# Kernel tuning notes

Hardware: AMD Instinct MI355X
Metric: run time of the kernel (lower is better)

## Reference

```python
import jax, jax.numpy as jnp
import numpy as np

BATCH = 4096
DIM = 256
TEMPERATURE = 0.5
EPS = 1e-8  # torch CosineSimilarity norm clamp


def setup_inputs() -> dict:
    key = jax.random.key(0)
    k1, k2 = jax.random.split(key)
    zA = jax.random.normal(k1, (BATCH, DIM), dtype=jnp.float32)
    zB = jax.random.normal(k2, (BATCH, DIM), dtype=jnp.float32)
    return {"zA": zA, "zB": zB}


def reference(zA, zB):
    b = zA.shape[0]
    N = 2 * b
    z = jnp.concatenate([zA, zB], axis=0)                      # [N, D]
    norm = jnp.maximum(jnp.linalg.norm(z, axis=1, keepdims=True), EPS)
    zn = z / norm
    # cosine-similarity matrix via normalize + GEMM (same math as the
    # broadcasted CosineSimilarity(dim=2) in the original)
    sim = (zn @ zn.T) / TEMPERATURE                            # [N, N]

    idx = jnp.arange(N)
    pos = sim[idx, (idx + b) % N]                              # diag(+b) ++ diag(-b)

    # CE with label 0 over logits=[pos, negatives]; the logit set per row is
    # exactly {all j != i} (pos partner included once), so mask only the diagonal.
    neg_inf = jnp.finfo(sim.dtype).min
    masked = jnp.where(jnp.eye(N, dtype=bool), neg_inf, sim)
    per_row = jax.nn.logsumexp(masked, axis=1) - pos           # [N]
    loss = jnp.sum(per_row) / N                                # reduction='sum' / N
    return loss
```

## Files before the change

### kernel.cpp

```cpp
#include <hip/hip_runtime.h>
#include <hip/hip_bf16.h>

#define N_ROWS 8192
#define BATCH 4096
#define DIM 256

#define NB 64
#define BR 128
#define CT 32
#define NT 4
#define NBLK (NB * (NB + 1) / 2)
#define TILEB (CT * 512)
#define KEXP 2.8853900817779268f

typedef __attribute__((ext_vector_type(8))) short bfrag8;
typedef __attribute__((ext_vector_type(4))) float facc4;

#define GLOAD_LDS16(g, l) __builtin_amdgcn_global_load_lds( \
    (const __attribute__((address_space(1))) unsigned int*)(g), \
    (__attribute__((address_space(3))) unsigned int*)(l), 16, 0, 0)

__global__ __launch_bounds__(256) void normalize_kernel(
    const float* __restrict__ zA, const float* __restrict__ zB,
    __hip_bfloat16* __restrict__ zn) {
    int tid = threadIdx.x;
    int wave = tid >> 6, lane = tid & 63;
    int row = blockIdx.x * 4 + wave;
    const float* src = (row < BATCH) ? (zA + (size_t)row * DIM)
                                     : (zB + (size_t)(row - BATCH) * DIM);
    float4 v = ((const float4*)src)[lane];
    float ss = v.x * v.x + v.y * v.y + v.z * v.z + v.w * v.w;
    #pragma unroll
    for (int m = 32; m; m >>= 1) ss += __shfl_xor(ss, m);
    float inv = 1.0f / fmaxf(sqrtf(ss), 1e-8f);
    union { ushort4 u; __hip_bfloat16 h[4]; } o;
    o.h[0] = __float2bfloat16(v.x * inv);
    o.h[1] = __float2bfloat16(v.y * inv);
    o.h[2] = __float2bfloat16(v.z * inv);
    o.h[3] = __float2bfloat16(v.w * inv);
    ((ushort4*)zn)[(size_t)row * (DIM / 4) + lane] = o.u;
}

__global__ __launch_bounds__(256, 3) void ntxent_main(
    const __hip_bfloat16* __restrict__ zn_,
    float* __restrict__ ep, float* __restrict__ pp) {
    const char* zn = (const char*)zn_;
    __shared__ char lds[2 * TILEB] __attribute__((aligned(1024)));
    __shared__ float colbuf[4][BR];
    int tid = threadIdx.x, lane = tid & 63, wave = tid >> 6;
    int quad = lane >> 4, l15 = lane & 15;

    int bid = blockIdx.x;
    int k = (bid & 7) * (NBLK / 8) + (bid >> 3);

    int bi = (int)(0.5f * (129.0f - sqrtf(16641.0f - 8.0f * (float)k)));
    if (bi < 0) bi = 0;
    if (bi > NB - 1) bi = NB - 1;
    while (bi * (129 - bi) / 2 > k) --bi;
    while ((bi + 1) * (128 - bi) / 2 <= k) ++bi;
    int bj = bi + (k - bi * (129 - bi) / 2);
    bool diagblk = (bi == bj);

    int row0 = bi * BR + wave * 32;
    const char* gBt = zn + (size_t)bj * BR * 512;

    int h = lane >> 5;
    int olane = (lane & 31) * 16;
    unsigned sofs[4];
    #pragma unroll
    for (int c = 0; c < 4; c++) {
        int col = wave * 8 + 2 * c + h;
        sofs[c] = (unsigned)(col * 512 + (olane ^ ((col & 7) << 4)));
    }

    #pragma unroll
    for (int c = 0; c < 4; c++)
        GLOAD_LDS16(gBt + sofs[c], lds + wave * 4096 + c * 1024);

    bfrag8 a[2][8];
    #pragma unroll
    for (int s = 0; s < 2; s++) {
        const char* ap = zn + (size_t)(row0 + s * 16 + l15) * 512 + quad * 16;
        #pragma unroll
        for (int ks = 0; ks < 8; ks++)
            a[s][ks] = *(const bfrag8*)(ap + ks * 64);
    }

    float es[2][4];
    #pragma unroll
    for (int s = 0; s < 2; s++)
        #pragma unroll
        for (int r = 0; r < 4; r++) es[s][r] = 0.f;

    __syncthreads();

    for (int t = 0; t < NT; t++) {
        char* cur = lds + (t & 1) * TILEB;
        char* nxt = lds + ((t + 1) & 1) * TILEB;
        if (t + 1 < NT) {
            const char* g = gBt + (size_t)(t + 1) * TILEB;
            #pragma unroll
            for (int c = 0; c < 4; c++)
                GLOAD_LDS16(g + sofs[c], nxt + wave * 4096 + c * 1024);
        }

        #pragma unroll
        for (int sub = 0; sub < 2; sub++) {
            int c2 = sub * 16 + l15;
            const char* bp = cur + c2 * 512;
            unsigned sw = (unsigned)((c2 & 7) << 4);
            bfrag8 bf[8];
            #pragma unroll
            for (int ks = 0; ks < 8; ks++) {
                unsigned o = (unsigned)(quad * 16 + ks * 64);
                bf[ks] = *(const bfrag8*)(bp + (o ^ sw));
            }

            facc4 acc[2];
            acc[0] = (facc4){0.f, 0.f, 0.f, 0.f};
            acc[1] = (facc4){0.f, 0.f, 0.f, 0.f};
            #pragma unroll
            for (int ks = 0; ks < 8; ks++) {
                acc[0] = __builtin_amdgcn_mfma_f32_16x16x32_bf16(a[0][ks], bf[ks], acc[0], 0, 0, 0);
                acc[1] = __builtin_amdgcn_mfma_f32_16x16x32_bf16(a[1][ks], bf[ks], acc[1], 0, 0, 0);
            }

            int ctile = bj * BR + t * CT + sub * 16;
            int gcol = ctile + l15;
            float ce = 0.0f;
            bool isdiag = (ctile >> 5) == (row0 >> 5);
            bool ispos  = (ctile >> 5) == ((row0 ^ BATCH) >> 5);

            if (isdiag) {
                #pragma unroll
                for (int s = 0; s < 2; s++)
                    #pragma unroll
                    for (int r = 0; r < 4; r++) {
                        int grow = row0 + s * 16 + quad * 4 + r;
                        float e = __builtin_amdgcn_exp2f(acc[s][r] * KEXP);
                        if (gcol == grow) e = 0.0f;
                        es[s][r] += e; ce += e;
                    }
            } else {
                #pragma unroll
                for (int s = 0; s < 2; s++)
                    #pragma unroll
                    for (int r = 0; r < 4; r++) {
                        float e = __builtin_amdgcn_exp2f(acc[s][r] * KEXP);
                        es[s][r] += e; ce += e;
                    }
                if (ispos) {
                    #pragma unroll
                    for (int s = 0; s < 2; s++)
                        #pragma unroll
                        for (int r = 0; r < 4; r++) {
                            int grow = row0 + s * 16 + quad * 4 + r;
                            if (gcol == (grow ^ BATCH)) {
                                float d = acc[s][r];
                                pp[grow] = d;
                                pp[grow ^ BATCH] = d;
                            }
                        }
                }
            }
            if (!diagblk) {
                ce += __shfl_xor(ce, 16);
                ce += __shfl_xor(ce, 32);
                if (lane < 16) colbuf[wave][t * CT + sub * 16 + l15] = ce;
            }
        }

        __syncthreads();
    }

    #pragma unroll
    for (int s = 0; s < 2; s++)
        #pragma unroll
        for (int r = 0; r < 4; r++) {
            float e = es[s][r];
            #pragma unroll
            for (int m = 1; m < 16; m <<= 1) e += __shfl_xor(e, m);
            if (l15 == 0)
                ep[(size_t)(row0 + s * 16 + quad * 4 + r) * NB + bj] = e;
        }

    if (!diagblk && tid < BR) {
        float v = colbuf[0][tid] + colbuf[1][tid] + colbuf[2][tid] + colbuf[3][tid];
        ep[(size_t)(bj * BR + tid) * NB + bi] = v;
    }
}

__global__ __launch_bounds__(256) void finalize_kernel(
    const float* __restrict__ ep, const float* __restrict__ pp,
    float* __restrict__ out) {
    int tid = threadIdx.x;
    int i = blockIdx.x * 256 + tid;
    const float4* epr = (const float4*)(ep + (size_t)i * NB);
    float e = 0.0f;
    #pragma unroll
    for (int s = 0; s < NB / 4; s++) {
        float4 v = epr[s];
        e += (v.x + v.y) + (v.z + v.w);
    }
    float v = __logf(e) - 2.0f * pp[i];
    #pragma unroll
    for (int m = 32; m; m >>= 1) v += __shfl_xor(v, m);
    __shared__ float wsum[4];
    if ((tid & 63) == 0) wsum[tid >> 6] = v;
    __syncthreads();
    if (tid == 0)
        atomicAdd(out, (wsum[0] + wsum[1] + wsum[2] + wsum[3]) * (1.0f / N_ROWS));
}

extern "C" void kernel_launch(void* const* d_in, const int* in_sizes, int n_in,
                              void* d_out, int out_size, void* d_ws, size_t ws_size,
                              hipStream_t stream) {
    const float* zA = (const float*)d_in[0];
    const float* zB = (const float*)d_in[1];
    float* out = (float*)d_out;
    char* ws = (char*)d_ws;
    __hip_bfloat16* zn = (__hip_bfloat16*)ws;
    float* ep = (float*)(ws + (size_t)N_ROWS * DIM * 2);
    float* pp = ep + (size_t)N_ROWS * NB;

    hipMemsetAsync(out, 0, sizeof(float), stream);
    normalize_kernel<<<N_ROWS / 4, 256, 0, stream>>>(zA, zB, zn);
    ntxent_main<<<NBLK, 256, 0, stream>>>(zn, ep, pp);
    finalize_kernel<<<N_ROWS / 256, 256, 0, stream>>>(ep, pp, out);
}
```

Measured before the change: 105.3 us.

## Split fused GEMM+exp reduction into GEMM writing exp tiles and separate sum kernel

The fused kernel did the row and column exp-sum reductions in registers and LDS. It now writes every 128x128 exp tile to a workspace buffer in global memory. A new kernel then reads each tile back and computes row and column sums into the partial-sum array. This drops the shuffle and LDS reduction work from the GEMM kernel. In exchange it writes and rereads about 2080*64KB (roughly 136MB) of intermediate data and adds one more kernel launch.

```diff
diff --git a/kernel.cpp b/kernel.cpp
--- a/kernel.cpp
+++ b/kernel.cpp
@@ -19,6 +19,15 @@
 #define GLOAD_LDS16(g, l) __builtin_amdgcn_global_load_lds( \
     (const __attribute__((address_space(1))) unsigned int*)(g), \
     (__attribute__((address_space(3))) unsigned int*)(l), 16, 0, 0)
+
+__device__ __forceinline__ void pair_decode(int k, int& bi, int& bj) {
+    bi = (int)(0.5f * (129.0f - sqrtf(16641.0f - 8.0f * (float)k)));
+    if (bi < 0) bi = 0;
+    if (bi > NB - 1) bi = NB - 1;
+    while (bi * (129 - bi) / 2 > k) --bi;
+    while ((bi + 1) * (128 - bi) / 2 <= k) ++bi;
+    bj = bi + (k - bi * (129 - bi) / 2);
+}
 
 __global__ __launch_bounds__(256) void normalize_kernel(
     const float* __restrict__ zA, const float* __restrict__ zB,
@@ -41,28 +50,23 @@
     ((ushort4*)zn)[(size_t)row * (DIM / 4) + lane] = o.u;
 }
 
-__global__ __launch_bounds__(256, 3) void ntxent_main(
+__global__ __launch_bounds__(256, 3) void ntxent_gemm(
     const __hip_bfloat16* __restrict__ zn_,
-    float* __restrict__ ep, float* __restrict__ pp) {
+    float* __restrict__ E, float* __restrict__ pp) {
     const char* zn = (const char*)zn_;
     __shared__ char lds[2 * TILEB] __attribute__((aligned(1024)));
-    __shared__ float colbuf[4][BR];
     int tid = threadIdx.x, lane = tid & 63, wave = tid >> 6;
     int quad = lane >> 4, l15 = lane & 15;
 
     int bid = blockIdx.x;
     int k = (bid & 7) * (NBLK / 8) + (bid >> 3);
-
-    int bi = (int)(0.5f * (129.0f - sqrtf(16641.0f - 8.0f * (float)k)));
-    if (bi < 0) bi = 0;
-    if (bi > NB - 1) bi = NB - 1;
-    while (bi * (129 - bi) / 2 > k) --bi;
-    while ((bi + 1) * (128 - bi) / 2 <= k) ++bi;
-    int bj = bi + (k - bi * (129 - bi) / 2);
+    int bi, bj; pair_decode(k, bi, bj);
     bool diagblk = (bi == bj);
+    bool posblk  = (bj == (bi ^ 32));
 
     int row0 = bi * BR + wave * 32;
     const char* gBt = zn + (size_t)bj * BR * 512;
+    float* Et = E + (size_t)k * (BR * BR);
 
     int h = lane >> 5;
     int olane = (lane & 31) * 16;
@@ -85,12 +89,6 @@
         for (int ks = 0; ks < 8; ks++)
             a[s][ks] = *(const bfrag8*)(ap + ks * 64);
     }
-
-    float es[2][4];
-    #pragma unroll
-    for (int s = 0; s < 2; s++)
-        #pragma unroll
-        for (int r = 0; r < 4; r++) es[s][r] = 0.f;
 
     __syncthreads();
 
@@ -125,68 +123,84 @@
                 acc[1] = __builtin_amdgcn_mfma_f32_16x16x32_bf16(a[1][ks], bf[ks], acc[1], 0, 0, 0);
             }
 
-            int ctile = bj * BR + t * CT + sub * 16;
-            int gcol = ctile + l15;
-            float ce = 0.0f;
-            bool isdiag = (ctile >> 5) == (row0 >> 5);
-            bool ispos  = (ctile >> 5) == ((row0 ^ BATCH) >> 5);
-
-            if (isdiag) {
-                #pragma unroll
-                for (int s = 0; s < 2; s++)
+            int C = t * CT + sub * 16 + l15;
+            #pragma unroll
+            for (int s = 0; s < 2; s++) {
+                int R0 = wave * 32 + s * 16 + quad * 4;
+                int dd = C - R0;
+                if (posblk) {
                     #pragma unroll
-                    for (int r = 0; r < 4; r++) {
-                        int grow = row0 + s * 16 + quad * 4 + r;
-                        float e = __builtin_amdgcn_exp2f(acc[s][r] * KEXP);
-                        if (gcol == grow) e = 0.0f;
-                        es[s][r] += e; ce += e;
-                    }
-            } else {
-                #pragma unroll
-                for (int s = 0; s < 2; s++)
-                    #pragma unroll
-                    for (int r = 0; r < 4; r++) {
-                        float e = __builtin_amdgcn_exp2f(acc[s][r] * KEXP);
-                        es[s][r] += e; ce += e;
-                    }
-                if (ispos) {
-                    #pragma unroll
-                    for (int s = 0; s < 2; s++)
-                        #pragma unroll
-                        for (int r = 0; r < 4; r++) {
-                            int grow = row0 + s * 16 + quad * 4 + r;
-                            if (gcol == (grow ^ BATCH)) {
-                                float d = acc[s][r];
-                                pp[grow] = d;
-                                pp[grow ^ BATCH] = d;
-                            }
+                    for (int r = 0; r < 4; r++)
+                        if (dd == r) {
+                            int grow = bi * BR + R0 + r;
+                            float d = acc[s][r];
+                            pp[grow] = d;
+                            pp[grow ^ BATCH] = d;
                         }
                 }
+                float e0 = __builtin_amdgcn_exp2f(acc[s][0] * KEXP);
+                float e1 = __builtin_amdgcn_exp2f(acc[s][1] * KEXP);
+                float e2 = __builtin_amdgcn_exp2f(acc[s][2] * KEXP);
+                float e3 = __builtin_amdgcn_exp2f(acc[s][3] * KEXP);
+                if (diagblk) {
+                    e0 = (dd == 0) ? 0.0f : e0;
+                    e1 = (dd == 1) ? 0.0f : e1;
+                    e2 = (dd == 2) ? 0.0f : e2;
+                    e3 = (dd == 3) ? 0.0f : e3;
+                }
+                *(float4*)(Et + (size_t)C * BR + R0) = make_float4(e0, e1, e2, e3);
             }
-            if (!diagblk) {
-                ce += __shfl_xor(ce, 16);
-                ce += __shfl_xor(ce, 32);
-                if (lane < 16) colbuf[wave][t * CT + sub * 16 + l15] = ce;
-            }
-        }
-
+        }
         __syncthreads();
     }
-
-    #pragma unroll
-    for (int s = 0; s < 2; s++)
-        #pragma unroll
-        for (int r = 0; r < 4; r++) {
-            float e = es[s][r];
-            #pragma unroll
-            for (int m = 1; m < 16; m <<= 1) e += __shfl_xor(e, m);
-            if (l15 == 0)
-                ep[(size_t)(row0 + s * 16 + quad * 4 + r) * NB + bj] = e;
-        }
-
-    if (!diagblk && tid < BR) {
-        float v = colbuf[0][tid] + colbuf[1][tid] + colbuf[2][tid] + colbuf[3][tid];
-        ep[(size_t)(bj * BR + tid) * NB + bi] = v;
+}
+
+__global__ __launch_bounds__(256) void ntxent_sums(
+    const float* __restrict__ E, float* __restrict__ ep) {
+    int bid = blockIdx.x;
+    int k = (bid & 7) * (NBLK / 8) + (bid >> 3);
+    int bi, bj; pair_decode(k, bi, bj);
+    bool diagblk = (bi == bj);
+    const float* T = E + (size_t)k * (BR * BR);
+    int tid = threadIdx.x;
+
+    {
+        int C = tid >> 1, h = tid & 1;
+        const float4* p = (const float4*)(T + (size_t)C * BR + h * 64);
+        float cs = 0.0f;
+        #pragma unroll
+        for (int i = 0; i < 16; i++) {
+            float4 v = p[i];
+            cs += (v.x + v.y) + (v.z + v.w);
+        }
+        cs += __shfl_xor(cs, 1);
+        if (!diagblk && h == 0)
+            ep[(size_t)(bj * BR + C) * NB + bi] = cs;
+    }
+
+    {
+        int rg = tid >> 3, cc = tid & 7;
+        float r0 = 0.f, r1 = 0.f, r2 = 0.f, r3 = 0.f;
+        #pragma unroll
+        for (int i = 0; i < 16; i++) {
+            int C = cc * 16 + i;
+            float4 v = *(const float4*)(T + (size_t)C * BR + rg * 4);
+            r0 += v.x; r1 += v.y; r2 += v.z; r3 += v.w;
+        }
+        #pragma unroll
+        for (int m = 1; m < 8; m <<= 1) {
+            r0 += __shfl_xor(r0, m);
+            r1 += __shfl_xor(r1, m);
+            r2 += __shfl_xor(r2, m);
+            r3 += __shfl_xor(r3, m);
+        }
+        if (cc == 0) {
+            size_t base = (size_t)(bi * BR + rg * 4) * NB + bj;
+            ep[base] = r0;
+            ep[base + NB] = r1;
+            ep[base + 2 * NB] = r2;
+            ep[base + 3 * NB] = r3;
+        }
     }
 }
 
@@ -222,9 +236,11 @@
     __hip_bfloat16* zn = (__hip_bfloat16*)ws;
     float* ep = (float*)(ws + (size_t)N_ROWS * DIM * 2);
     float* pp = ep + (size_t)N_ROWS * NB;
+    float* E  = (float*)(ws + ((size_t)8 << 20));
 
     hipMemsetAsync(out, 0, sizeof(float), stream);
     normalize_kernel<<<N_ROWS / 4, 256, 0, stream>>>(zA, zB, zn);
-    ntxent_main<<<NBLK, 256, 0, stream>>>(zn, ep, pp);
+    ntxent_gemm<<<NBLK, 256, 0, stream>>>(zn, E, pp);
+    ntxent_sums<<<NBLK, 256, 0, stream>>>(E, ep);
     finalize_kernel<<<N_ROWS / 256, 256, 0, stream>>>(ep, pp, out);
 }
```

Result: slower. 152.6 us (+45.0%).

## Use 256x128 rectangular tiles over symmetric similarity triangle with paired row-band scheduling

Applied to the files above, without the earlier changes.

Each block now covers 256 rows by 128 columns instead of 128x128. Each wave holds 64 rows of A fragments in registers, so every LDS-loaded B fragment feeds four MFMAs instead of two. Blocks are scheduled as paired row bands to balance the triangular work, and the finalize kernel sums only the valid per-band partial entries. This raises register use, so occupancy drops from 3 to 2 blocks per CU, and the diagonal and positive-pair masking become per-element index checks.

```diff
diff --git a/kernel.cpp b/kernel.cpp
--- a/kernel.cpp
+++ b/kernel.cpp
@@ -5,11 +5,13 @@
 #define BATCH 4096
 #define DIM 256
 
-#define NB 64
-#define BR 128
+#define NP 32
+#define PR 256
+#define CW 128
+#define NJ 64
 #define CT 32
 #define NT 4
-#define NBLK (NB * (NB + 1) / 2)
+#define NBLK 1056
 #define TILEB (CT * 512)
 #define KEXP 2.8853900817779268f
 
@@ -41,54 +43,56 @@
     ((ushort4*)zn)[(size_t)row * (DIM / 4) + lane] = o.u;
 }
 
-__global__ __launch_bounds__(256, 3) void ntxent_main(
+__global__ __launch_bounds__(256, 2) void ntxent_main(
     const __hip_bfloat16* __restrict__ zn_,
     float* __restrict__ ep, float* __restrict__ pp) {
     const char* zn = (const char*)zn_;
     __shared__ char lds[2 * TILEB] __attribute__((aligned(1024)));
-    __shared__ float colbuf[4][BR];
+    __shared__ float colbuf[4][CW];
     int tid = threadIdx.x, lane = tid & 63, wave = tid >> 6;
     int quad = lane >> 4, l15 = lane & 15;
 
     int bid = blockIdx.x;
     int k = (bid & 7) * (NBLK / 8) + (bid >> 3);
 
-    int bi = (int)(0.5f * (129.0f - sqrtf(16641.0f - 8.0f * (float)k)));
-    if (bi < 0) bi = 0;
-    if (bi > NB - 1) bi = NB - 1;
-    while (bi * (129 - bi) / 2 > k) --bi;
-    while ((bi + 1) * (128 - bi) / 2 <= k) ++bi;
-    int bj = bi + (k - bi * (129 - bi) / 2);
-    bool diagblk = (bi == bj);
-
-    int row0 = bi * BR + wave * 32;
-    const char* gBt = zn + (size_t)bj * BR * 512;
+    int m = k / 66, c = k % 66;
+    int n0 = 64 - 2 * m;
+    int p, j;
+    if (c < n0) { p = m;      j = 2 * m + c; }
+    else        { p = 31 - m; j = 2 * p + (c - n0); }
+
+    int jp = j >> 1, jd = j & 1;
+    bool diagband = (jp == p);
+    bool posband  = (jp == (p ^ 16));
+
+    int row0 = p * PR + wave * 64;
+    const char* gBt = zn + (size_t)j * CW * 512;
 
     int h = lane >> 5;
     int olane = (lane & 31) * 16;
     unsigned sofs[4];
     #pragma unroll
-    for (int c = 0; c < 4; c++) {
-        int col = wave * 8 + 2 * c + h;
-        sofs[c] = (unsigned)(col * 512 + (olane ^ ((col & 7) << 4)));
-    }
-
-    #pragma unroll
-    for (int c = 0; c < 4; c++)
-        GLOAD_LDS16(gBt + sofs[c], lds + wave * 4096 + c * 1024);
-
-    bfrag8 a[2][8];
-    #pragma unroll
-    for (int s = 0; s < 2; s++) {
+    for (int cc = 0; cc < 4; cc++) {
+        int col = wave * 8 + 2 * cc + h;
+        sofs[cc] = (unsigned)(col * 512 + (olane ^ ((col & 7) << 4)));
+    }
+
+    #pragma unroll
+    for (int cc = 0; cc < 4; cc++)
+        GLOAD_LDS16(gBt + sofs[cc], lds + wave * 4096 + cc * 1024);
+
+    bfrag8 a[4][8];
+    #pragma unroll
+    for (int s = 0; s < 4; s++) {
         const char* ap = zn + (size_t)(row0 + s * 16 + l15) * 512 + quad * 16;
         #pragma unroll
         for (int ks = 0; ks < 8; ks++)
             a[s][ks] = *(const bfrag8*)(ap + ks * 64);
     }
 
-    float es[2][4];
-    #pragma unroll
-    for (int s = 0; s < 2; s++)
+    float es[4][4];
+    #pragma unroll
+    for (int s = 0; s < 4; s++)
         #pragma unroll
         for (int r = 0; r < 4; r++) es[s][r] = 0.f;
 
@@ -100,8 +104,8 @@
         if (t + 1 < NT) {
             const char* g = gBt + (size_t)(t + 1) * TILEB;
             #pragma unroll
-            for (int c = 0; c < 4; c++)
-                GLOAD_LDS16(g + sofs[c], nxt + wave * 4096 + c * 1024);
+            for (int cc = 0; cc < 4; cc++)
+                GLOAD_LDS16(g + sofs[cc], nxt + wave * 4096 + cc * 1024);
         }
 
         #pragma unroll
@@ -116,54 +120,38 @@
                 bf[ks] = *(const bfrag8*)(bp + (o ^ sw));
             }
 
-            facc4 acc[2];
-            acc[0] = (facc4){0.f, 0.f, 0.f, 0.f};
-            acc[1] = (facc4){0.f, 0.f, 0.f, 0.f};
-            #pragma unroll
-            for (int ks = 0; ks < 8; ks++) {
-                acc[0] = __builtin_amdgcn_mfma_f32_16x16x32_bf16(a[0][ks], bf[ks], acc[0], 0, 0, 0);
-                acc[1] = __builtin_amdgcn_mfma_f32_16x16x32_bf16(a[1][ks], bf[ks], acc[1], 0, 0, 0);
-            }
-
-            int ctile = bj * BR + t * CT + sub * 16;
-            int gcol = ctile + l15;
+            facc4 acc[4];
+            #pragma unroll
+            for (int s = 0; s < 4; s++) acc[s] = (facc4){0.f, 0.f, 0.f, 0.f};
+            #pragma unroll
+            for (int ks = 0; ks < 8; ks++)
+                #pragma unroll
+                for (int s = 0; s < 4; s++)
+                    acc[s] = __builtin_amdgcn_mfma_f32_16x16x32_bf16(a[s][ks], bf[ks], acc[s], 0, 0, 0);
+
+            int C = t * CT + sub * 16 + l15;
             float ce = 0.0f;
-            bool isdiag = (ctile >> 5) == (row0 >> 5);
-            bool ispos  = (ctile >> 5) == ((row0 ^ BATCH) >> 5);
-
-            if (isdiag) {
-                #pragma unroll
-                for (int s = 0; s < 2; s++)
+            #pragma unroll
+            for (int s = 0; s < 4; s++) {
+                int dd = C + 128 * jd - (wave * 64 + s * 16 + quad * 4);
+                if (posband) {
                     #pragma unroll
-                    for (int r = 0; r < 4; r++) {
-                        int grow = row0 + s * 16 + quad * 4 + r;
-                        float e = __builtin_amdgcn_exp2f(acc[s][r] * KEXP);
-                        if (gcol == grow) e = 0.0f;
-                        es[s][r] += e; ce += e;
-                    }
-            } else {
-                #pragma unroll
-                for (int s = 0; s < 2; s++)
-                    #pragma unroll
-                    for (int r = 0; r < 4; r++) {
-                        float e = __builtin_amdgcn_exp2f(acc[s][r] * KEXP);
-                        es[s][r] += e; ce += e;
-                    }
-                if (ispos) {
-                    #pragma unroll
-                    for (int s = 0; s < 2; s++)
-                        #pragma unroll
-                        for (int r = 0; r < 4; r++) {
+                    for (int r = 0; r < 4; r++)
+                        if (dd == r) {
                             int grow = row0 + s * 16 + quad * 4 + r;
-                            if (gcol == (grow ^ BATCH)) {
-                                float d = acc[s][r];
-                                pp[grow] = d;
-                                pp[grow ^ BATCH] = d;
-                            }
+                            float d = acc[s][r];
+                            pp[grow] = d;
+                            pp[grow ^ BATCH] = d;
                         }
                 }
+                #pragma unroll
+                for (int r = 0; r < 4; r++) {
+                    float e = __builtin_amdgcn_exp2f(acc[s][r] * KEXP);
+                    if (diagband && dd == r) e = 0.0f;
+                    es[s][r] += e; ce += e;
+                }
             }
-            if (!diagblk) {
+            if (!diagband) {
                 ce += __shfl_xor(ce, 16);
                 ce += __shfl_xor(ce, 32);
                 if (lane < 16) colbuf[wave][t * CT + sub * 16 + l15] = ce;
@@ -174,19 +162,19 @@
     }
 
     #pragma unroll
-    for (int s = 0; s < 2; s++)
+    for (int s = 0; s < 4; s++)
         #pragma unroll
         for (int r = 0; r < 4; r++) {
             float e = es[s][r];
             #pragma unroll
-            for (int m = 1; m < 16; m <<= 1) e += __shfl_xor(e, m);
+            for (int mm = 1; mm < 16; mm <<= 1) e += __shfl_xor(e, mm);
             if (l15 == 0)
-                ep[(size_t)(row0 + s * 16 + quad * 4 + r) * NB + bj] = e;
+                ep[(size_t)(row0 + s * 16 + quad * 4 + r) * NJ + j] = e;
         }
 
-    if (!diagblk && tid < BR) {
+    if (!diagband && tid < CW) {
         float v = colbuf[0][tid] + colbuf[1][tid] + colbuf[2][tid] + colbuf[3][tid];
-        ep[(size_t)(bj * BR + tid) * NB + bi] = v;
+        ep[(size_t)(j * CW + tid) * NJ + p] = v;
     }
 }
 
@@ -195,16 +183,14 @@
     float* __restrict__ out) {
     int tid = threadIdx.x;
     int i = blockIdx.x * 256 + tid;
-    const float4* epr = (const float4*)(ep + (size_t)i * NB);
+    int p = blockIdx.x;
+    const float* epr = ep + (size_t)i * NJ;
     float e = 0.0f;
-    #pragma unroll
-    for (int s = 0; s < NB / 4; s++) {
-        float4 v = epr[s];
-        e += (v.x + v.y) + (v.z + v.w);
-    }
+    for (int s = 0; s < p; s++) e += epr[s];
+    for (int s = 2 * p; s < NJ; s++) e += epr[s];
     float v = __logf(e) - 2.0f * pp[i];
     #pragma unroll
-    for (int m = 32; m; m >>= 1) v += __shfl_xor(v, m);
+    for (int mm = 32; mm; mm >>= 1) v += __shfl_xor(v, mm);
     __shared__ float wsum[4];
     if ((tid & 63) == 0) wsum[tid >> 6] = v;
     __syncthreads();
@@ -221,7 +207,7 @@
     char* ws = (char*)d_ws;
     __hip_bfloat16* zn = (__hip_bfloat16*)ws;
     float* ep = (float*)(ws + (size_t)N_ROWS * DIM * 2);
-    float* pp = ep + (size_t)N_ROWS * NB;
+    float* pp = ep + (size_t)N_ROWS * NJ;
 
     hipMemsetAsync(out, 0, sizeof(float), stream);
     normalize_kernel<<<N_ROWS / 4, 256, 0, stream>>>(zA, zB, zn);
```

Result: slower. 116.3 us (+10.5%).
